# Performance work log

Hardware: AMD Instinct MI355X
Metric: run time of the kernel (lower is better)

The kernel has to match this reference:

```python
import jax, jax.numpy as jnp
import numpy as np

N, C, NIRR, E = 2048, 128, 9, 10          # nodes, channels, sum(2l+1) of input irreps, num elements
DOUT = (1, 3)                              # output irrep dims for 128x0e + 128x1o
K3, K2, K1 = 4, 3, 2                       # number of CG paths per correlation order


def setup_inputs() -> dict:
    key = jax.random.key(0)
    ks = jax.random.split(key, 24)
    inp = {
        'node_feats': jax.random.normal(ks[0], (N, C, NIRR), jnp.float32),
        'node_attrs': jax.nn.one_hot(jax.random.randint(ks[1], (N,), 0, E), E, dtype=jnp.float32),
        'sc': jax.random.normal(ks[2], (N, C * sum(DOUT)), jnp.float32),
    }
    i = 3
    for li, d in enumerate(DOUT):
        # U tensors: fixed (buffer) generalized CG coupling tensors; sparse in e3nn,
        # here random dense stand-ins with the exact same shapes / contraction structure.
        inp[f'u3_l{li}'] = 0.1 * jax.random.normal(ks[i + 0], (d, NIRR, NIRR, NIRR, K3), jnp.float32)
        inp[f'u2_l{li}'] = 0.1 * jax.random.normal(ks[i + 1], (d, NIRR, NIRR, K2), jnp.float32)
        inp[f'u1_l{li}'] = 0.1 * jax.random.normal(ks[i + 2], (d, NIRR, K1), jnp.float32)
        s3, s2, s1 = 1.0 / np.sqrt(K3 * C), 1.0 / np.sqrt(K2 * C), 1.0 / np.sqrt(K1 * C)
        inp[f'w3_l{li}'] = s3 * jax.random.normal(ks[i + 3], (E, K3, C), jnp.float32)
        inp[f'w2_l{li}'] = s2 * jax.random.normal(ks[i + 4], (E, K2, C), jnp.float32)
        inp[f'w1_l{li}'] = s1 * jax.random.normal(ks[i + 5], (E, K1, C), jnp.float32)
        i += 6
    inp['lin_w0'] = jax.random.normal(ks[i], (C, C), jnp.float32)
    inp['lin_w1'] = jax.random.normal(ks[i + 1], (C, C), jnp.float32)
    return inp


def _contraction(x, y, u3, u2, u1, w3, w2, w1):
    # MACE Contraction: correlation-3 nested CG contraction for one output irrep.
    # x: [N,C,n], y: [N,E] one-hot, u_nu: [d, n*nu, k_nu], w_nu: [E, k_nu, C]
    wk3 = jnp.einsum('ekc,be->bkc', w3, y)                       # per-node path weights
    out = jnp.einsum('dpqik,bkc,bci->bcdpq', u3, wk3, x)         # main, nu=3
    out = jnp.einsum('dpik,ekc,be->bcdpi', u2, w2, y) + out      # add nu=2 weights
    out = jnp.einsum('bcdpi,bci->bcdp', out, x)                  # contract one feature index
    out = jnp.einsum('dik,ekc,be->bcdi', u1, w1, y) + out        # add nu=1 weights
    out = jnp.einsum('bcdi,bci->bcd', out, x)                    # [N,C,d]
    return out


def reference(node_feats, node_attrs, sc,
              u3_l0, u2_l0, u1_l0, w3_l0, w2_l0, w1_l0,
              u3_l1, u2_l1, u1_l1, w3_l1, w2_l1, w1_l1,
              lin_w0, lin_w1):
    f0 = _contraction(node_feats, node_attrs, u3_l0, u2_l0, u1_l0, w3_l0, w2_l0, w1_l0)  # [N,C,1]
    f1 = _contraction(node_feats, node_attrs, u3_l1, u2_l1, u1_l1, w3_l1, w2_l1, w1_l1)  # [N,C,3]
    inv_sqrt_c = 1.0 / np.sqrt(C).astype(np.float32)
    # o3.Linear: block-diagonal channel mixing per irrep, 1/sqrt(fan_in) normalization
    o0 = jnp.einsum('bim,ij->bjm', f0, lin_w0) * inv_sqrt_c
    o1 = jnp.einsum('bim,ij->bjm', f1, lin_w1) * inv_sqrt_c
    out = jnp.concatenate([o0.reshape(o0.shape[0], -1), o1.reshape(o1.shape[0], -1)], axis=-1)
    return out + sc
```

## Files before the change

kernel.cpp:

```cpp
#include <hip/hip_runtime.h>

#define N_NODES 2048
#define C_CH    128
#define NIRR    9
#define E_EL    10

#define NS3 165
#define NS2 45
#define US3_FLOATS (NS3 * 16)
#define US2_FLOATS (NS2 * 16)
#define US1_FLOATS (9 * 8)

typedef float pf2 __attribute__((ext_vector_type(2)));

struct Tab {
    unsigned char pairP[NS2], pairQ[NS2];
    unsigned char triPair[NS3], triI[NS3];
};
constexpr Tab makeTab() {
    Tab t{};
    int s2 = 0, s3 = 0;
    for (int p = 0; p < 9; p++)
        for (int q = p; q < 9; q++) {
            t.pairP[s2] = (unsigned char)p;
            t.pairQ[s2] = (unsigned char)q;
            for (int i = q; i < 9; i++) {
                t.triPair[s3] = (unsigned char)s2;
                t.triI[s3] = (unsigned char)i;
                s3++;
            }
            s2++;
        }
    return t;
}
constexpr Tab TAB = makeTab();

__global__ __launch_bounds__(256) void build_sym_kernel(
    const float* __restrict__ u3_l0, const float* __restrict__ u2_l0, const float* __restrict__ u1_l0,
    const float* __restrict__ u3_l1, const float* __restrict__ u2_l1, const float* __restrict__ u1_l1,
    float* __restrict__ us3, float* __restrict__ us2, float* __restrict__ us1)
{
    int t = blockIdx.x * 256 + threadIdx.x;
    if (t < US3_FLOATS) {
        int k = t & 3;
        int rs = t >> 2;
        int s = rs % NS3;
        int ds = rs / NS3;
        int pp = 0, qq = 0, ii = 0, cntr = 0;
        for (int p = 0; p < 9; p++)
            for (int q = p; q < 9; q++)
                for (int i = q; i < 9; i++) {
                    if (cntr == s) { pp = p; qq = q; ii = i; }
                    cntr++;
                }
        const float* u = (ds == 0) ? u3_l0 : (u3_l1 + (ds - 1) * 2916);
        int perm[6][3] = {{pp,qq,ii},{pp,ii,qq},{qq,pp,ii},{qq,ii,pp},{ii,pp,qq},{ii,qq,pp}};
        float acc = 0.f;
        #pragma unroll
        for (int j = 0; j < 6; j++)
            acc += u[((perm[j][0] * 9 + perm[j][1]) * 9 + perm[j][2]) * 4 + k];
        float mult = (pp == qq && qq == ii) ? 6.f : ((pp == qq || qq == ii) ? 2.f : 1.f);
        us3[ds * (NS3 * 4) + s * 4 + k] = acc / mult;
    } else if (t < US3_FLOATS + US2_FLOATS) {
        int t2 = t - US3_FLOATS;
        int k = t2 & 3;
        int rs = t2 >> 2;
        int s = rs % NS2;
        int ds = rs / NS2;
        float v = 0.f;
        if (k < 3) {
            int pp = 0, qq = 0, cntr = 0;
            for (int p = 0; p < 9; p++)
                for (int q = p; q < 9; q++) {
                    if (cntr == s) { pp = p; qq = q; }
                    cntr++;
                }
            const float* u = (ds == 0) ? u2_l0 : (u2_l1 + (ds - 1) * 243);
            float acc = u[(pp * 9 + qq) * 3 + k] + u[(qq * 9 + pp) * 3 + k];
            v = (pp == qq) ? acc * 0.5f : acc;
        }
        us2[ds * (NS2 * 4) + s * 4 + k] = v;
    } else if (t < US3_FLOATS + US2_FLOATS + US1_FLOATS) {
        int t1 = t - US3_FLOATS - US2_FLOATS;
        int p = t1 >> 3, dk = t1 & 7, ds = dk >> 1, k = dk & 1;
        const float* u = (ds == 0) ? u1_l0 : (u1_l1 + (ds - 1) * 18);
        us1[ds * 18 + p * 2 + k] = u[p * 2 + k];
    }
}

__global__ __launch_bounds__(512, 4) void fused_kernel(
    const float* __restrict__ x, const float* __restrict__ y,
    const float* __restrict__ us3, const float* __restrict__ us2, const float* __restrict__ us1,
    const float* __restrict__ w3_l0, const float* __restrict__ w2_l0, const float* __restrict__ w1_l0,
    const float* __restrict__ w3_l1, const float* __restrict__ w2_l1, const float* __restrict__ w1_l1,
    const float* __restrict__ lw0, const float* __restrict__ lw1,
    const float* __restrict__ sc, float* __restrict__ out)
{
    __shared__ float fs[4][132];
    int tid = threadIdx.x;
    int c = tid & 127;
    int r = __builtin_amdgcn_readfirstlane(tid >> 7);
    int b = blockIdx.x;

    int e = 0;
    #pragma unroll
    for (int k = 1; k < E_EL; k++)
        if (y[b * E_EL + k] > 0.5f) e = k;
    e = __builtin_amdgcn_readfirstlane(e);

    float xv[9];
    {
        const float* xp = x + ((size_t)b * C_CH + c) * NIRR;
        #pragma unroll
        for (int i = 0; i < 9; i++) xv[i] = xp[i];
    }

    const float* t3 = us3 + r * (NS3 * 4);
    const float* t2 = us2 + r * (NS2 * 4);
    const float* t1 = us1 + r * 18;
    const pf2* T3v = (const pf2*)t3;
    const pf2* T2v = (const pf2*)t2;
    const pf2* T1v = (const pf2*)t1;

    pf2 G3a = {0.f, 0.f}, G3b = {0.f, 0.f};
    pf2 G2a = {0.f, 0.f};
    float G2c = 0.f;
    pf2 G1v = {0.f, 0.f};

    #pragma unroll
    for (int p = 0; p < 9; p++) {
        pf2 xpv = {xv[p], xv[p]};
        G1v = __builtin_elementwise_fma(T1v[p], xpv, G1v);
    }

    float pq = 0.f;
    #pragma unroll
    for (int s = 0; s < NS3; s++) {
        const int pi = TAB.triPair[s];
        if (s == 0 || TAB.triPair[s] != TAB.triPair[s - 1]) {
            pq = xv[TAB.pairP[pi]] * xv[TAB.pairQ[pi]];
            pf2 pqv = {pq, pq};
            G2a = __builtin_elementwise_fma(T2v[pi * 2], pqv, G2a);
            G2c = __builtin_fmaf(t2[pi * 4 + 2], pq, G2c);
        }
        float X = pq * xv[TAB.triI[s]];
        pf2 Xv = {X, X};
        G3a = __builtin_elementwise_fma(T3v[s * 2], Xv, G3a);
        G3b = __builtin_elementwise_fma(T3v[s * 2 + 1], Xv, G3b);
    }

    float G3[4] = {G3a.x, G3a.y, G3b.x, G3b.y};
    float G2[3] = {G2a.x, G2a.y, G2c};
    float G1[2] = {G1v.x, G1v.y};

    float acc = 0.f;
    if (r == 0) {
        #pragma unroll
        for (int k = 0; k < 4; k++) acc += w3_l0[(e * 4 + k) * 128 + c] * G3[k];
        #pragma unroll
        for (int k = 0; k < 3; k++) acc += w2_l0[(e * 3 + k) * 128 + c] * G2[k];
        #pragma unroll
        for (int k = 0; k < 2; k++) acc += w1_l0[(e * 2 + k) * 128 + c] * G1[k];
    } else {
        #pragma unroll
        for (int k = 0; k < 4; k++) acc += w3_l1[(e * 4 + k) * 128 + c] * G3[k];
        #pragma unroll
        for (int k = 0; k < 3; k++) acc += w2_l1[(e * 3 + k) * 128 + c] * G2[k];
        #pragma unroll
        for (int k = 0; k < 2; k++) acc += w1_l1[(e * 2 + k) * 128 + c] * G1[k];
    }
    fs[r][c] = acc;
    __syncthreads();

    if (tid < 128) {
        int sel, m = 0, j0;
        const float4* W4;
        bool isl0 = (tid < 32);
        if (isl0) { sel = 0; j0 = 4 * tid; W4 = (const float4*)lw0; }
        else {
            int idx = tid - 32;
            m = idx >> 5;
            j0 = 4 * (idx & 31);
            sel = 1 + m;
            W4 = (const float4*)lw1;
        }
        int wbase = j0 >> 2;

        float a0 = 0.f, a1 = 0.f, a2 = 0.f, a3 = 0.f;
        #pragma unroll 4
        for (int ib = 0; ib < 32; ib++) {
            float4 f = *(const float4*)&fs[sel][4 * ib];
            float4 w0 = W4[(4 * ib + 0) * 32 + wbase];
            float4 w1 = W4[(4 * ib + 1) * 32 + wbase];
            float4 w2 = W4[(4 * ib + 2) * 32 + wbase];
            float4 w3 = W4[(4 * ib + 3) * 32 + wbase];
            a0 += f.x * w0.x + f.y * w1.x + f.z * w2.x + f.w * w3.x;
            a1 += f.x * w0.y + f.y * w1.y + f.z * w2.y + f.w * w3.y;
            a2 += f.x * w0.z + f.y * w1.z + f.z * w2.z + f.w * w3.z;
            a3 += f.x * w0.w + f.y * w1.w + f.z * w2.w + f.w * w3.w;
        }

        const float inv_sqrt_c = 0.08838834764831845f;
        if (isl0) {
            size_t o = (size_t)b * 512 + j0;
            float4 s = *(const float4*)(sc + o);
            float4 rr;
            rr.x = a0 * inv_sqrt_c + s.x;
            rr.y = a1 * inv_sqrt_c + s.y;
            rr.z = a2 * inv_sqrt_c + s.z;
            rr.w = a3 * inv_sqrt_c + s.w;
            *(float4*)(out + o) = rr;
        } else {
            float av[4] = {a0, a1, a2, a3};
            #pragma unroll
            for (int jj = 0; jj < 4; jj++) {
                size_t o = (size_t)b * 512 + 128 + 3 * (j0 + jj) + m;
                out[o] = av[jj] * inv_sqrt_c + sc[o];
            }
        }
    }
}

extern "C" void kernel_launch(void* const* d_in, const int* in_sizes, int n_in,
                              void* d_out, int out_size, void* d_ws, size_t ws_size,
                              hipStream_t stream) {
    const float* x     = (const float*)d_in[0];
    const float* y     = (const float*)d_in[1];
    const float* sc    = (const float*)d_in[2];
    const float* u3_l0 = (const float*)d_in[3];
    const float* u2_l0 = (const float*)d_in[4];
    const float* u1_l0 = (const float*)d_in[5];
    const float* w3_l0 = (const float*)d_in[6];
    const float* w2_l0 = (const float*)d_in[7];
    const float* w1_l0 = (const float*)d_in[8];
    const float* u3_l1 = (const float*)d_in[9];
    const float* u2_l1 = (const float*)d_in[10];
    const float* u1_l1 = (const float*)d_in[11];
    const float* w3_l1 = (const float*)d_in[12];
    const float* w2_l1 = (const float*)d_in[13];
    const float* w1_l1 = (const float*)d_in[14];
    const float* lw0   = (const float*)d_in[15];
    const float* lw1   = (const float*)d_in[16];
    float* out = (float*)d_out;

    float* us3 = (float*)d_ws;
    float* us2 = us3 + US3_FLOATS;
    float* us1 = us2 + US2_FLOATS;

    int tot = US3_FLOATS + US2_FLOATS + US1_FLOATS;
    build_sym_kernel<<<(tot + 255) / 256, 256, 0, stream>>>(
        u3_l0, u2_l0, u1_l0, u3_l1, u2_l1, u1_l1, us3, us2, us1);
    fused_kernel<<<N_NODES, 512, 0, stream>>>(
        x, y, us3, us2, us1,
        w3_l0, w2_l0, w1_l0, w3_l1, w2_l1, w1_l1,
        lw0, lw1, sc, out);
}
```

Before: 132.9 us.

## Process two nodes per block to reuse symmetric CG coefficient loads

Each block now handles two nodes instead of one, so every loaded coefficient from the symmetric U tables feeds FMAs for both nodes, and twice as many threads take part in the output linear stage. The aim is to halve the per-node cost of coefficient loads and raise the FMA-to-load ratio. In exchange, register pressure roughly doubles under launch_bounds(512,4), which risks spills or lower occupancy, and the grid is halved to 1024 blocks.

```diff
diff --git a/kernel.cpp b/kernel.cpp
--- a/kernel.cpp
+++ b/kernel.cpp
@@ -96,23 +96,27 @@
     const float* __restrict__ lw0, const float* __restrict__ lw1,
     const float* __restrict__ sc, float* __restrict__ out)
 {
-    __shared__ float fs[4][132];
+    __shared__ float fs[2][4][132];
     int tid = threadIdx.x;
     int c = tid & 127;
     int r = __builtin_amdgcn_readfirstlane(tid >> 7);
-    int b = blockIdx.x;
-
-    int e = 0;
+    int b0 = blockIdx.x * 2;
+
+    int e0 = 0, e1 = 0;
     #pragma unroll
-    for (int k = 1; k < E_EL; k++)
-        if (y[b * E_EL + k] > 0.5f) e = k;
-    e = __builtin_amdgcn_readfirstlane(e);
-
-    float xv[9];
+    for (int k = 1; k < E_EL; k++) {
+        if (y[b0 * E_EL + k] > 0.5f) e0 = k;
+        if (y[(b0 + 1) * E_EL + k] > 0.5f) e1 = k;
+    }
+    e0 = __builtin_amdgcn_readfirstlane(e0);
+    e1 = __builtin_amdgcn_readfirstlane(e1);
+
+    float xv0[9], xv1[9];
     {
-        const float* xp = x + ((size_t)b * C_CH + c) * NIRR;
-        #pragma unroll
-        for (int i = 0; i < 9; i++) xv[i] = xp[i];
+        const float* xp0 = x + ((size_t)b0 * C_CH + c) * NIRR;
+        const float* xp1 = x + ((size_t)(b0 + 1) * C_CH + c) * NIRR;
+        #pragma unroll
+        for (int i = 0; i < 9; i++) { xv0[i] = xp0[i]; xv1[i] = xp1[i]; }
     }
 
     const float* t3 = us3 + r * (NS3 * 4);
@@ -122,63 +126,89 @@
     const pf2* T2v = (const pf2*)t2;
     const pf2* T1v = (const pf2*)t1;
 
-    pf2 G3a = {0.f, 0.f}, G3b = {0.f, 0.f};
-    pf2 G2a = {0.f, 0.f};
-    float G2c = 0.f;
-    pf2 G1v = {0.f, 0.f};
+    pf2 G3a0 = {0.f, 0.f}, G3b0 = {0.f, 0.f}, G3a1 = {0.f, 0.f}, G3b1 = {0.f, 0.f};
+    pf2 G2a0 = {0.f, 0.f}, G2a1 = {0.f, 0.f};
+    float G2c0 = 0.f, G2c1 = 0.f;
+    pf2 G1v0 = {0.f, 0.f}, G1v1 = {0.f, 0.f};
 
     #pragma unroll
     for (int p = 0; p < 9; p++) {
-        pf2 xpv = {xv[p], xv[p]};
-        G1v = __builtin_elementwise_fma(T1v[p], xpv, G1v);
-    }
-
-    float pq = 0.f;
+        pf2 u1v = T1v[p];
+        pf2 xa = {xv0[p], xv0[p]};
+        pf2 xb = {xv1[p], xv1[p]};
+        G1v0 = __builtin_elementwise_fma(u1v, xa, G1v0);
+        G1v1 = __builtin_elementwise_fma(u1v, xb, G1v1);
+    }
+
+    float pq0 = 0.f, pq1 = 0.f;
     #pragma unroll
     for (int s = 0; s < NS3; s++) {
         const int pi = TAB.triPair[s];
         if (s == 0 || TAB.triPair[s] != TAB.triPair[s - 1]) {
-            pq = xv[TAB.pairP[pi]] * xv[TAB.pairQ[pi]];
-            pf2 pqv = {pq, pq};
-            G2a = __builtin_elementwise_fma(T2v[pi * 2], pqv, G2a);
-            G2c = __builtin_fmaf(t2[pi * 4 + 2], pq, G2c);
-        }
-        float X = pq * xv[TAB.triI[s]];
-        pf2 Xv = {X, X};
-        G3a = __builtin_elementwise_fma(T3v[s * 2], Xv, G3a);
-        G3b = __builtin_elementwise_fma(T3v[s * 2 + 1], Xv, G3b);
-    }
-
-    float G3[4] = {G3a.x, G3a.y, G3b.x, G3b.y};
-    float G2[3] = {G2a.x, G2a.y, G2c};
-    float G1[2] = {G1v.x, G1v.y};
-
-    float acc = 0.f;
-    if (r == 0) {
-        #pragma unroll
-        for (int k = 0; k < 4; k++) acc += w3_l0[(e * 4 + k) * 128 + c] * G3[k];
-        #pragma unroll
-        for (int k = 0; k < 3; k++) acc += w2_l0[(e * 3 + k) * 128 + c] * G2[k];
-        #pragma unroll
-        for (int k = 0; k < 2; k++) acc += w1_l0[(e * 2 + k) * 128 + c] * G1[k];
-    } else {
-        #pragma unroll
-        for (int k = 0; k < 4; k++) acc += w3_l1[(e * 4 + k) * 128 + c] * G3[k];
-        #pragma unroll
-        for (int k = 0; k < 3; k++) acc += w2_l1[(e * 3 + k) * 128 + c] * G2[k];
-        #pragma unroll
-        for (int k = 0; k < 2; k++) acc += w1_l1[(e * 2 + k) * 128 + c] * G1[k];
-    }
-    fs[r][c] = acc;
+            pq0 = xv0[TAB.pairP[pi]] * xv0[TAB.pairQ[pi]];
+            pq1 = xv1[TAB.pairP[pi]] * xv1[TAB.pairQ[pi]];
+            pf2 u2v = T2v[pi * 2];
+            float u2c = t2[pi * 4 + 2];
+            pf2 pa = {pq0, pq0};
+            pf2 pb = {pq1, pq1};
+            G2a0 = __builtin_elementwise_fma(u2v, pa, G2a0);
+            G2a1 = __builtin_elementwise_fma(u2v, pb, G2a1);
+            G2c0 = __builtin_fmaf(u2c, pq0, G2c0);
+            G2c1 = __builtin_fmaf(u2c, pq1, G2c1);
+        }
+        float X0 = pq0 * xv0[TAB.triI[s]];
+        float X1 = pq1 * xv1[TAB.triI[s]];
+        pf2 ua = T3v[s * 2];
+        pf2 ub = T3v[s * 2 + 1];
+        pf2 Xa = {X0, X0};
+        pf2 Xb = {X1, X1};
+        G3a0 = __builtin_elementwise_fma(ua, Xa, G3a0);
+        G3b0 = __builtin_elementwise_fma(ub, Xa, G3b0);
+        G3a1 = __builtin_elementwise_fma(ua, Xb, G3a1);
+        G3b1 = __builtin_elementwise_fma(ub, Xb, G3b1);
+    }
+
+    const float* W3 = (r == 0) ? w3_l0 : w3_l1;
+    const float* W2 = (r == 0) ? w2_l0 : w2_l1;
+    const float* W1 = (r == 0) ? w1_l0 : w1_l1;
+    {
+        float G3n0[4] = {G3a0.x, G3a0.y, G3b0.x, G3b0.y};
+        float G3n1[4] = {G3a1.x, G3a1.y, G3b1.x, G3b1.y};
+        float G2n0[3] = {G2a0.x, G2a0.y, G2c0};
+        float G2n1[3] = {G2a1.x, G2a1.y, G2c1};
+        float G1n0[2] = {G1v0.x, G1v0.y};
+        float G1n1[2] = {G1v1.x, G1v1.y};
+        float acc0 = 0.f, acc1 = 0.f;
+        #pragma unroll
+        for (int k = 0; k < 4; k++) {
+            acc0 += W3[(e0 * 4 + k) * 128 + c] * G3n0[k];
+            acc1 += W3[(e1 * 4 + k) * 128 + c] * G3n1[k];
+        }
+        #pragma unroll
+        for (int k = 0; k < 3; k++) {
+            acc0 += W2[(e0 * 3 + k) * 128 + c] * G2n0[k];
+            acc1 += W2[(e1 * 3 + k) * 128 + c] * G2n1[k];
+        }
+        #pragma unroll
+        for (int k = 0; k < 2; k++) {
+            acc0 += W1[(e0 * 2 + k) * 128 + c] * G1n0[k];
+            acc1 += W1[(e1 * 2 + k) * 128 + c] * G1n1[k];
+        }
+        fs[0][r][c] = acc0;
+        fs[1][r][c] = acc1;
+    }
     __syncthreads();
 
-    if (tid < 128) {
+    if (tid < 256) {
+        int n = tid >> 7;
+        int t = tid & 127;
+        int b = b0 + n;
         int sel, m = 0, j0;
         const float4* W4;
-        bool isl0 = (tid < 32);
-        if (isl0) { sel = 0; j0 = 4 * tid; W4 = (const float4*)lw0; }
+        bool isl0 = (t < 32);
+        if (isl0) { sel = 0; j0 = 4 * t; W4 = (const float4*)lw0; }
         else {
-            int idx = tid - 32;
+            int idx = t - 32;
             m = idx >> 5;
             j0 = 4 * (idx & 31);
             sel = 1 + m;
@@ -189,7 +219,7 @@
         float a0 = 0.f, a1 = 0.f, a2 = 0.f, a3 = 0.f;
         #pragma unroll 4
         for (int ib = 0; ib < 32; ib++) {
-            float4 f = *(const float4*)&fs[sel][4 * ib];
+            float4 f = *(const float4*)&fs[n][sel][4 * ib];
             float4 w0 = W4[(4 * ib + 0) * 32 + wbase];
             float4 w1 = W4[(4 * ib + 1) * 32 + wbase];
             float4 w2 = W4[(4 * ib + 2) * 32 + wbase];
@@ -250,7 +280,7 @@
     int tot = US3_FLOATS + US2_FLOATS + US1_FLOATS;
     build_sym_kernel<<<(tot + 255) / 256, 256, 0, stream>>>(
         u3_l0, u2_l0, u1_l0, u3_l1, u2_l1, u1_l1, us3, us2, us1);
-    fused_kernel<<<N_NODES, 512, 0, stream>>>(
+    fused_kernel<<<N_NODES / 2, 512, 0, stream>>>(
         x, y, us3, us2, us1,
         w3_l0, w2_l0, w1_l0, w3_l1, w2_l1, w1_l1,
         lw0, lw1, sc, out);
```

Measured after the change: 134.4 us. Within noise of the previous version (+1.1%).

## Split symmetric contraction terms across two thread halves with shared-memory reduction

Applied to the files above, without the earlier changes.

Doubles the block to 1024 threads. Each output-irrep role is split into two halves, and each half accumulates part of the nu=3, nu=2 and nu=1 symmetric terms. The partial G values are written to shared memory and summed before the per-element weight contraction. This shortens the serial FMA chain per thread, at the cost of an extra barrier, about 38KB of shared memory per block, redundant x loads, and possibly fewer resident blocks per CU.

```diff
diff --git a/kernel.cpp b/kernel.cpp
--- a/kernel.cpp
+++ b/kernel.cpp
@@ -10,6 +10,10 @@
 #define US3_FLOATS (NS3 * 16)
 #define US2_FLOATS (NS2 * 16)
 #define US1_FLOATS (9 * 8)
+
+#define S3_SPLIT 83
+#define S2_SPLIT 23
+#define P1_SPLIT 5
 
 typedef float pf2 __attribute__((ext_vector_type(2)));
 
@@ -88,7 +92,7 @@
     }
 }
 
-__global__ __launch_bounds__(512, 4) void fused_kernel(
+__global__ __launch_bounds__(1024, 2) void fused_kernel(
     const float* __restrict__ x, const float* __restrict__ y,
     const float* __restrict__ us3, const float* __restrict__ us2, const float* __restrict__ us1,
     const float* __restrict__ w3_l0, const float* __restrict__ w2_l0, const float* __restrict__ w1_l0,
@@ -96,10 +100,13 @@
     const float* __restrict__ lw0, const float* __restrict__ lw1,
     const float* __restrict__ sc, float* __restrict__ out)
 {
+    __shared__ float part[8 * 9 * 132];
     __shared__ float fs[4][132];
     int tid = threadIdx.x;
     int c = tid & 127;
-    int r = __builtin_amdgcn_readfirstlane(tid >> 7);
+    int role = __builtin_amdgcn_readfirstlane(tid >> 7);
+    int ds = role & 3;
+    int h = role >> 2;
     int b = blockIdx.x;
 
     int e = 0;
@@ -115,9 +122,9 @@
         for (int i = 0; i < 9; i++) xv[i] = xp[i];
     }
 
-    const float* t3 = us3 + r * (NS3 * 4);
-    const float* t2 = us2 + r * (NS2 * 4);
-    const float* t1 = us1 + r * 18;
+    const float* t3 = us3 + ds * (NS3 * 4);
+    const float* t2 = us2 + ds * (NS2 * 4);
+    const float* t1 = us1 + ds * 18;
     const pf2* T3v = (const pf2*)t3;
     const pf2* T2v = (const pf2*)t2;
     const pf2* T1v = (const pf2*)t1;
@@ -127,49 +134,88 @@
     float G2c = 0.f;
     pf2 G1v = {0.f, 0.f};
 
-    #pragma unroll
-    for (int p = 0; p < 9; p++) {
-        pf2 xpv = {xv[p], xv[p]};
-        G1v = __builtin_elementwise_fma(T1v[p], xpv, G1v);
-    }
-
-    float pq = 0.f;
-    #pragma unroll
-    for (int s = 0; s < NS3; s++) {
-        const int pi = TAB.triPair[s];
-        if (s == 0 || TAB.triPair[s] != TAB.triPair[s - 1]) {
-            pq = xv[TAB.pairP[pi]] * xv[TAB.pairQ[pi]];
-            pf2 pqv = {pq, pq};
-            G2a = __builtin_elementwise_fma(T2v[pi * 2], pqv, G2a);
-            G2c = __builtin_fmaf(t2[pi * 4 + 2], pq, G2c);
-        }
-        float X = pq * xv[TAB.triI[s]];
-        pf2 Xv = {X, X};
-        G3a = __builtin_elementwise_fma(T3v[s * 2], Xv, G3a);
-        G3b = __builtin_elementwise_fma(T3v[s * 2 + 1], Xv, G3b);
-    }
-
-    float G3[4] = {G3a.x, G3a.y, G3b.x, G3b.y};
-    float G2[3] = {G2a.x, G2a.y, G2c};
-    float G1[2] = {G1v.x, G1v.y};
-
-    float acc = 0.f;
-    if (r == 0) {
-        #pragma unroll
-        for (int k = 0; k < 4; k++) acc += w3_l0[(e * 4 + k) * 128 + c] * G3[k];
-        #pragma unroll
-        for (int k = 0; k < 3; k++) acc += w2_l0[(e * 3 + k) * 128 + c] * G2[k];
-        #pragma unroll
-        for (int k = 0; k < 2; k++) acc += w1_l0[(e * 2 + k) * 128 + c] * G1[k];
+    if (h == 0) {
+        #pragma unroll
+        for (int p = 0; p < P1_SPLIT; p++) {
+            pf2 xpv = {xv[p], xv[p]};
+            G1v = __builtin_elementwise_fma(T1v[p], xpv, G1v);
+        }
+        #pragma unroll
+        for (int s2 = 0; s2 < S2_SPLIT; s2++) {
+            float pq2 = xv[TAB.pairP[s2]] * xv[TAB.pairQ[s2]];
+            pf2 pqv = {pq2, pq2};
+            G2a = __builtin_elementwise_fma(T2v[s2 * 2], pqv, G2a);
+            G2c = __builtin_fmaf(t2[s2 * 4 + 2], pq2, G2c);
+        }
+        float pq = 0.f;
+        #pragma unroll
+        for (int s = 0; s < S3_SPLIT; s++) {
+            const int pi = TAB.triPair[s];
+            if (s == 0 || TAB.triPair[s] != TAB.triPair[s - 1])
+                pq = xv[TAB.pairP[pi]] * xv[TAB.pairQ[pi]];
+            float X = pq * xv[TAB.triI[s]];
+            pf2 Xv = {X, X};
+            G3a = __builtin_elementwise_fma(T3v[s * 2], Xv, G3a);
+            G3b = __builtin_elementwise_fma(T3v[s * 2 + 1], Xv, G3b);
+        }
     } else {
         #pragma unroll
-        for (int k = 0; k < 4; k++) acc += w3_l1[(e * 4 + k) * 128 + c] * G3[k];
-        #pragma unroll
-        for (int k = 0; k < 3; k++) acc += w2_l1[(e * 3 + k) * 128 + c] * G2[k];
-        #pragma unroll
-        for (int k = 0; k < 2; k++) acc += w1_l1[(e * 2 + k) * 128 + c] * G1[k];
-    }
-    fs[r][c] = acc;
+        for (int p = P1_SPLIT; p < 9; p++) {
+            pf2 xpv = {xv[p], xv[p]};
+            G1v = __builtin_elementwise_fma(T1v[p], xpv, G1v);
+        }
+        #pragma unroll
+        for (int s2 = S2_SPLIT; s2 < NS2; s2++) {
+            float pq2 = xv[TAB.pairP[s2]] * xv[TAB.pairQ[s2]];
+            pf2 pqv = {pq2, pq2};
+            G2a = __builtin_elementwise_fma(T2v[s2 * 2], pqv, G2a);
+            G2c = __builtin_fmaf(t2[s2 * 4 + 2], pq2, G2c);
+        }
+        float pq = 0.f;
+        #pragma unroll
+        for (int s = S3_SPLIT; s < NS3; s++) {
+            const int pi = TAB.triPair[s];
+            if (s == S3_SPLIT || TAB.triPair[s] != TAB.triPair[s - 1])
+                pq = xv[TAB.pairP[pi]] * xv[TAB.pairQ[pi]];
+            float X = pq * xv[TAB.triI[s]];
+            pf2 Xv = {X, X};
+            G3a = __builtin_elementwise_fma(T3v[s * 2], Xv, G3a);
+            G3b = __builtin_elementwise_fma(T3v[s * 2 + 1], Xv, G3b);
+        }
+    }
+
+    {
+        float G[9] = {G3a.x, G3a.y, G3b.x, G3b.y, G2a.x, G2a.y, G2c, G1v.x, G1v.y};
+        #pragma unroll
+        for (int k = 0; k < 9; k++)
+            part[(role * 9 + k) * 132 + c] = G[k];
+    }
+    __syncthreads();
+
+    if (tid < 512) {
+        float G[9];
+        #pragma unroll
+        for (int k = 0; k < 9; k++)
+            G[k] = part[(role * 9 + k) * 132 + c] + part[((role + 4) * 9 + k) * 132 + c];
+
+        float acc = 0.f;
+        if (role == 0) {
+            #pragma unroll
+            for (int k = 0; k < 4; k++) acc += w3_l0[(e * 4 + k) * 128 + c] * G[k];
+            #pragma unroll
+            for (int k = 0; k < 3; k++) acc += w2_l0[(e * 3 + k) * 128 + c] * G[4 + k];
+            #pragma unroll
+            for (int k = 0; k < 2; k++) acc += w1_l0[(e * 2 + k) * 128 + c] * G[7 + k];
+        } else {
+            #pragma unroll
+            for (int k = 0; k < 4; k++) acc += w3_l1[(e * 4 + k) * 128 + c] * G[k];
+            #pragma unroll
+            for (int k = 0; k < 3; k++) acc += w2_l1[(e * 3 + k) * 128 + c] * G[4 + k];
+            #pragma unroll
+            for (int k = 0; k < 2; k++) acc += w1_l1[(e * 2 + k) * 128 + c] * G[7 + k];
+        }
+        fs[role][c] = acc;
+    }
     __syncthreads();
 
     if (tid < 128) {
@@ -250,7 +296,7 @@
     int tot = US3_FLOATS + US2_FLOATS + US1_FLOATS;
     build_sym_kernel<<<(tot + 255) / 256, 256, 0, stream>>>(
         u3_l0, u2_l0, u1_l0, u3_l1, u2_l1, u1_l1, us3, us2, us1);
-    fused_kernel<<<N_NODES, 512, 0, stream>>>(
+    fused_kernel<<<N_NODES, 1024, 0, stream>>>(
         x, y, us3, us2, us1,
         w3_l0, w2_l0, w1_l0, w3_l1, w2_l1, w1_l1,
         lw0, lw1, sc, out);
```

Result: slower. 139.9 us (+5.3%).
